# Performance work log

Hardware: AMD Instinct MI355X
Metric: run time of the kernel (lower is better)

Reference implementation:

```python
import jax, jax.numpy as jnp
import numpy as np

B = 4; N_LIG = 150; N_PROT = 550; N = 700
H = 128; HEADS = 4; KPH = 32; HPH = 32
L = 6; K = 48; EDGE_CH = 128; CUTOFF = 10.0
PROT_F = 27; NUM_CLASSES = 13
LOG2 = 0.6931471805599453
FLAT = N * H  # 89600, matches fc1 in_features


def ssp(x):
    # ShiftedSoftplus
    return jax.nn.softplus(x) - LOG2


def lin(x, w, b):
    # torch Linear convention: w is [out, in]
    return jnp.einsum('...i,oi->...o', x, w) + b


def setup_inputs() -> dict:
    key = jax.random.key(0)
    ki = iter(jax.random.split(key, 40))

    def nrm(shape, fan_in):
        return jax.random.normal(next(ki), shape, jnp.float32) / np.sqrt(fan_in).astype(np.float32)

    lig_pos = jax.random.normal(next(ki), (B, N_LIG, 3), jnp.float32) * 3.0
    lig_t = jax.random.randint(next(ki), (B, N_LIG, 1), 0, NUM_CLASSES).astype(jnp.float32)
    state = jnp.concatenate([lig_pos, lig_t], axis=-1)  # [B, N_LIG, 4]
    protein_pos_v = jnp.concatenate([
        jax.random.normal(next(ki), (B, N_PROT, 3), jnp.float32) * 3.0,
        jax.random.normal(next(ki), (B, N_PROT, PROT_F), jnp.float32)], axis=-1)  # [B, N_PROT, 30]

    inp = dict(state=state, protein_pos_v=protein_pos_v)
    inp['w_prot'] = nrm((H, PROT_F), PROT_F); inp['b_prot'] = jnp.zeros((H,), jnp.float32)
    inp['w_lig'] = nrm((H, NUM_CLASSES), NUM_CLASSES); inp['b_lig'] = jnp.zeros((H,), jnp.float32)
    # per-layer stacked encoder params (grouped 1x1 conv == per-head linear, no bias)
    inp['wq'] = nrm((L, HEADS, KPH, HPH), HPH)
    inp['wk'] = nrm((L, HEADS, KPH, HPH), HPH)
    inp['wv'] = nrm((L, HEADS, HPH, HPH), HPH)
    inp['wkn1_w'] = nrm((L, KPH, EDGE_CH), EDGE_CH); inp['wkn1_b'] = jnp.zeros((L, KPH), jnp.float32)
    inp['wkn2_w'] = nrm((L, KPH, KPH), KPH); inp['wkn2_b'] = jnp.zeros((L, KPH), jnp.float32)
    inp['wkl_w'] = nrm((L, KPH, KPH), KPH); inp['wkl_b'] = jnp.zeros((L, KPH), jnp.float32)
    inp['wvn1_w'] = nrm((L, HPH, EDGE_CH), EDGE_CH); inp['wvn1_b'] = jnp.zeros((L, HPH), jnp.float32)
    inp['wvn2_w'] = nrm((L, HPH, HPH), HPH); inp['wvn2_b'] = jnp.zeros((L, HPH), jnp.float32)
    inp['wvl_w'] = nrm((L, HPH, HPH), HPH); inp['wvl_b'] = jnp.zeros((L, HPH), jnp.float32)
    inp['cen_w'] = nrm((L, H, H), H); inp['cen_b'] = jnp.zeros((L, H), jnp.float32)
    inp['out_w'] = nrm((L, H, H), H); inp['out_b'] = jnp.zeros((L, H), jnp.float32)
    inp['ln_g'] = jnp.ones((L, H), jnp.float32); inp['ln_b'] = jnp.zeros((L, H), jnp.float32)
    inp['fc1_w'] = nrm((128, FLAT), FLAT); inp['fc1_b'] = jnp.zeros((128,), jnp.float32)
    inp['fc2_w'] = nrm((64, 128), 128); inp['fc2_b'] = jnp.zeros((64,), jnp.float32)
    inp['fc3_w'] = nrm((1, 64), 64); inp['fc3_b'] = jnp.zeros((1,), jnp.float32)
    return inp


def reference(state, protein_pos_v, w_prot, b_prot, w_lig, b_lig, wq, wk, wv,
              wkn1_w, wkn1_b, wkn2_w, wkn2_b, wkl_w, wkl_b,
              wvn1_w, wvn1_b, wvn2_w, wvn2_b, wvl_w, wvl_b,
              cen_w, cen_b, out_w, out_b, ln_g, ln_b,
              fc1_w, fc1_b, fc2_w, fc2_b, fc3_w, fc3_b):
    lig_pos = state[..., :3]
    lig_t = jax.lax.stop_gradient(state[..., 3]).astype(jnp.int32)
    lig_oh = jax.nn.one_hot(lig_t, NUM_CLASSES, dtype=jnp.float32)
    prot_pos = protein_pos_v[..., :3]
    prot_v = protein_pos_v[..., 3:]
    # compose_context: stable sort by batch -> protein atoms then ligand atoms per complex
    h = jnp.concatenate([lin(prot_v, w_prot, b_prot), lin(lig_oh, w_lig, b_lig)], axis=1)  # [B,N,H]
    pos = jnp.concatenate([prot_pos, lig_pos], axis=1)  # [B,N,3]
    # kNN graph (k nearest neighbors, no self loops), batched per complex
    d2 = jnp.sum((pos[:, :, None, :] - pos[:, None, :, :]) ** 2, axis=-1)  # [B,N,N]
    d2 = d2 + jnp.eye(N, dtype=d2.dtype) * 1e9
    _, nbr = jax.lax.top_k(-d2, K)  # [B,N,K]
    dist = jnp.sqrt(jnp.take_along_axis(d2, nbr, axis=2))  # [B,N,K]
    # Gaussian smearing of edge lengths
    offset = jnp.linspace(0.0, CUTOFF, EDGE_CH)
    coeff = -0.5 / (offset[1] - offset[0]) ** 2
    edge_attr = jnp.exp(coeff * (dist[..., None] - offset) ** 2)  # [B,N,K,E]
    gat = jax.vmap(lambda a, i: a[i])  # per-batch neighbor gather
    for l in range(L):
        xh = h.reshape(B, N, HEADS, HPH)
        q = jnp.einsum('bnhd,hkd->bnhk', xh, wq[l])
        kx = jnp.einsum('bnhd,hkd->bnhk', xh, wk[l])
        vx = jnp.einsum('bnhd,hkd->bnhk', xh, wv[l])
        w_k = lin(ssp(lin(edge_attr, wkn1_w[l], wkn1_b[l])), wkn2_w[l], wkn2_b[l])  # [B,N,K,KPH]
        keys_j = lin(w_k[:, :, :, None, :] * gat(kx, nbr), wkl_w[l], wkl_b[l])  # [B,N,K,heads,KPH]
        qk = jnp.einsum('bnhk,bnmhk->bnmh', q, keys_j)  # per-edge attention logits
        alpha = jax.nn.softmax(qk, axis=2)  # scatter_softmax over each node's K edges
        w_v = lin(ssp(lin(edge_attr, wvn1_w[l], wvn1_b[l])), wvn2_w[l], wvn2_b[l])  # [B,N,K,HPH]
        msg = lin(w_v[:, :, :, None, :] * gat(vx, nbr), wvl_w[l], wvl_b[l])  # [B,N,K,heads,HPH]
        aggr = jnp.einsum('bnmh,bnmhd->bnhd', alpha, msg).reshape(B, N, H)
        x = lin(h, cen_w[l], cen_b[l]) + aggr
        mu = jnp.mean(x, axis=-1, keepdims=True)
        var = jnp.var(x, axis=-1, keepdims=True)
        x = (x - mu) / jnp.sqrt(var + 1e-5) * ln_g[l] + ln_b[l]
        h = h + lin(ssp(x), out_w[l], out_b[l])  # residual per interaction block
    # decoup_batch + pad_tensor: constant 700 nodes/complex -> plain reshape
    x = h.reshape(B, FLAT)
    x = jax.nn.relu(lin(x, fc1_w, fc1_b))
    x = jax.nn.relu(lin(x, fc2_w, fc2_b))
    return lin(x, fc3_w, fc3_b)  # [B,1]
```

## Files before the change

### kernel.cpp

```cpp
#include <hip/hip_runtime.h>
#include <hip/hip_fp16.h>
#include <math.h>

constexpr int cB   = 4;
constexpr int cNL  = 150;
constexpr int cNP  = 550;
constexpr int cN   = 700;
constexpr int cH   = 128;
constexpr int cHeads = 4;
constexpr int cL   = 6;
constexpr int cK   = 48;
constexpr int cPF  = 27;
constexpr int cNC  = 13;
constexpr int cFLAT = cN * cH;
constexpr int cEdges = cB * cN * cK;

constexpr int   TABN = 4096;
#define TAB_DMAX 11.0f
#define TAB_HT   (TAB_DMAX / (float)(TABN - 1))
#define TAB_INV  ((float)(TABN - 1) / TAB_DMAX)

#define RBF_STEP (10.0f / 127.0f)
#define RBF_COEFF (-0.5f / (RBF_STEP * RBF_STEP))
#define LOG2F_C 0.69314718055994530942f

__device__ __forceinline__ float sspf(float x) {
    float ax = fabsf(x);
    return fmaxf(x, 0.0f) + __logf(1.0f + __expf(-ax)) - LOG2F_C;
}

__device__ __forceinline__ int mbcnt64(unsigned long long m) {
    return __builtin_amdgcn_mbcnt_hi((unsigned)(m >> 32),
           __builtin_amdgcn_mbcnt_lo((unsigned)m, 0));
}

__global__ void __launch_bounds__(256) k_init(
    const float* __restrict__ wq, const float* __restrict__ wk, const float* __restrict__ wv,
    const float* __restrict__ wkn1_w, const float* __restrict__ wvn1_w,
    const float* __restrict__ wkn2_w, const float* __restrict__ wvn2_w,
    const float* __restrict__ wvl_w,
    const float* __restrict__ cen_w, const float* __restrict__ out_w,
    float* __restrict__ wqT, float* __restrict__ wkT, float* __restrict__ wvT,
    float* __restrict__ w1Tk, float* __restrict__ w1Tv,
    float* __restrict__ w2Tk, float* __restrict__ w2Tv,
    float* __restrict__ wvlT,
    float* __restrict__ cenT, float* __restrict__ outT,
    const float* __restrict__ state, const float* __restrict__ ppv,
    const float* __restrict__ w_prot, const float* __restrict__ b_prot,
    const float* __restrict__ w_lig, const float* __restrict__ b_lig,
    float* __restrict__ h, float* __restrict__ pos)
{
    if (blockIdx.x < 1320) {
        int idx = blockIdx.x * 256 + threadIdx.x;
        if (idx < 3 * 24576) {
            int seg = idx / 24576, i = idx % 24576;
            const float* src = seg == 0 ? wq : (seg == 1 ? wk : wv);
            float* dst = seg == 0 ? wqT : (seg == 1 ? wkT : wvT);
            int l = i / 4096, r = i % 4096;
            int hh = r / 1024, r2 = r % 1024;
            int d = r2 / 32, k = r2 % 32;
            dst[i] = src[(((size_t)l * 4 + hh) * 32 + k) * 32 + d];
            return;
        }
        idx -= 3 * 24576;
        if (idx < 2 * 24576) {
            int seg = idx / 24576, i = idx % 24576;
            const float* src = seg == 0 ? wkn1_w : wvn1_w;
            float* dst = seg == 0 ? w1Tk : w1Tv;
            int l = i / 4096, r = i % 4096;
            int c = r / 32, o = r % 32;
            dst[i] = src[((size_t)l * 32 + o) * 128 + c];
            return;
        }
        idx -= 2 * 24576;
        if (idx < 3 * 6144) {
            int seg = idx / 6144, i = idx % 6144;
            const float* src = seg == 0 ? wkn2_w : (seg == 1 ? wvn2_w : wvl_w);
            float* dst = seg == 0 ? w2Tk : (seg == 1 ? w2Tv : wvlT);
            int l = i / 1024, r = i % 1024;
            int c = r / 32, o = r % 32;
            dst[i] = src[((size_t)l * 32 + o) * 32 + c];
            return;
        }
        idx -= 3 * 6144;
        int seg = idx / 98304, i = idx % 98304;
        const float* src = seg == 0 ? cen_w : out_w;
        float* dst = seg == 0 ? cenT : outT;
        int l = i / 16384, r = i % 16384;
        int ii = r / 128, o = r % 128;
        dst[i] = src[((size_t)l * 128 + o) * 128 + ii];
        return;
    }
    int rel = blockIdx.x - 1320;
    int node = rel * 2 + (threadIdx.x >> 7);
    int b = node / cN, n = node % cN;
    int o = threadIdx.x & 127;
    int lane = threadIdx.x & 63;
    float out;
    if (n < cNP) {
        const float* src = ppv + ((size_t)b * cNP + n) * 30;
        float v = (lane < 30) ? src[lane] : 0.f;
        float s = b_prot[o];
        #pragma unroll
        for (int f = 0; f < cPF; f++) s += w_prot[o * cPF + f] * __shfl(v, 3 + f);
        out = s;
        if (o < 3) pos[((size_t)b * cN + n) * 3 + o] = v;
    } else {
        int nl = n - cNP;
        const float* src = state + ((size_t)b * cNL + nl) * 4;
        float v = (lane < 4) ? src[lane] : 0.f;
        int t = (int)__shfl(v, 3);
        out = w_lig[o * cNC + t] + b_lig[o];
        if (o < 3) pos[((size_t)b * cN + n) * 3 + o] = v;
    }
    h[((size_t)b * cN + n) * cH + o] = out;
}

__global__ void __launch_bounds__(256) k_knn(
    const float* __restrict__ pos, int* __restrict__ nbr, float* __restrict__ dist,
    const float* __restrict__ w1Tk, const float* __restrict__ wkn1_b,
    const float* __restrict__ w2Tk, const float* __restrict__ wkn2_b,
    const float* __restrict__ w1Tv, const float* __restrict__ wvn1_b,
    const float* __restrict__ w2Tv, const float* __restrict__ wvn2_b,
    float* __restrict__ tabP,
    const float* __restrict__ hbuf,
    const float* __restrict__ wqT, const float* __restrict__ wkT, const float* __restrict__ wvT,
    float* __restrict__ q0, __half* __restrict__ kx0, __half* __restrict__ vx0)
{
    int tid = threadIdx.x;
    if (blockIdx.x < cN) {
        int lane = tid & 63;
        int node = blockIdx.x * 4 + (tid >> 6);
        int b = node / cN, n = node % cN;
        const float* pb = pos + (size_t)b * cN * 3;
        float px = pb[n * 3 + 0], py = pb[n * 3 + 1], pz = pb[n * 3 + 2];
        float d2v[11];
        #pragma unroll
        for (int s = 0; s < 11; s++) {
            int j = lane + s * 64;
            float d2 = 1e30f;
            if (j < cN) {
                float dx = pb[j * 3 + 0] - px;
                float dy = pb[j * 3 + 1] - py;
                float dz = pb[j * 3 + 2] - pz;
                d2 = dx * dx + dy * dy + dz * dz;
                if (j == n) d2 = 1e9f;
            }
            d2v[s] = d2;
        }
        unsigned p = 0;
        for (int bit = 30; bit >= 0; --bit) {
            unsigned t = p | (1u << bit);
            int cnt = 0;
            #pragma unroll
            for (int s = 0; s < 11; s++)
                cnt += __popcll(__ballot(__float_as_uint(d2v[s]) < t));
            if (cnt <= 47) p = t;
        }
        int c_lt = 0;
        #pragma unroll
        for (int s = 0; s < 11; s++)
            c_lt += __popcll(__ballot(__float_as_uint(d2v[s]) < p));
        int base = 0, ebase = c_lt, need = 48 - c_lt;
        #pragma unroll
        for (int s = 0; s < 11; s++) {
            unsigned u = __float_as_uint(d2v[s]);
            unsigned long long blt = __ballot(u < p);
            unsigned long long beq = __ballot(u == p);
            int posn = -1;
            int bl = mbcnt64(blt);
            if (u < p) posn = base + bl;
            base += __popcll(blt);
            int r = mbcnt64(beq);
            int cs = __popcll(beq);
            int take = need < cs ? need : cs;
            if (u == p && r < take) posn = ebase + r;
            ebase += take; need -= take;
            if (posn >= 0) {
                nbr[(size_t)node * cK + posn] = s * 64 + lane;
                dist[(size_t)node * cK + posn] = sqrtf(d2v[s]);
            }
        }
        return;
    }
    if (blockIdx.x < cN + TABN / 4) {
        int rel = blockIdx.x - cN;
        int lane = tid & 63;
        int e = rel * 4 + (tid >> 6);
        int side = lane >> 5, o = lane & 31;
        float d = (float)e * TAB_HT;
        float z = d * (127.0f / 10.0f);
        int c0 = (int)floorf(z) - 7;
        c0 = c0 < 0 ? 0 : (c0 > 112 ? 112 : c0);
        int i = lane & 15;
        float tt = d - RBF_STEP * (float)(c0 + i);
        float eav = __expf(RBF_COEFF * tt * tt);
        const float* w1T = (side ? w1Tv : w1Tk);
        const float* b1  = (side ? wvn1_b : wkn1_b);
        const float* w2T = (side ? w2Tv : w2Tk);
        const float* b2  = (side ? wvn2_b : wkn2_b);
        int srcb = side * 32;
        for (int l = 0; l < cL; l++) {
            float s = b1[l * 32 + o];
            const float* w1p = w1T + (size_t)l * 4096;
            #pragma unroll
            for (int ii = 0; ii < 16; ii++)
                s += w1p[(c0 + ii) * 32 + o] * __shfl(eav, ii);
            float t1 = sspf(s);
            float s2 = b2[l * 32 + o];
            const float* w2p = w2T + (size_t)l * 1024;
            #pragma unroll
            for (int cc = 0; cc < 32; cc++)
                s2 += w2p[cc * 32 + o] * __shfl(t1, srcb + cc);
            tabP[((((size_t)l * TABN + e) * 2 + side) * 32 + o) * 2] = s2;
            if (e > 0)
                tabP[((((size_t)l * TABN + (e - 1)) * 2 + side) * 32 + o) * 2 + 1] = s2;
        }
        return;
    }
    int bn = (blockIdx.x - cN - TABN / 4) * 2 + (tid >> 7);
    int o = tid & 127;
    int hh = o >> 5, kq = o & 31;
    float hval = hbuf[(size_t)bn * cH + o];
    size_t wo = ((size_t)0 * 4 + hh) * 1024;
    const float* bq = wqT + wo;
    const float* bk = wkT + wo;
    const float* bv = wvT + wo;
    int srcb = (hh & 1) * 32;
    float sq = 0.f, sk = 0.f, sv = 0.f;
    #pragma unroll
    for (int d = 0; d < 32; d++) {
        float x = __shfl(hval, srcb + d);
        sq += bq[d * 32 + kq] * x;
        sk += bk[d * 32 + kq] * x;
        sv += bv[d * 32 + kq] * x;
    }
    q0[(size_t)bn * cH + o] = sq;
    kx0[(size_t)bn * cH + o] = __float2half(sk);
    vx0[(size_t)bn * cH + o] = __float2half(sv);
}

__global__ void __launch_bounds__(128) k_attn(
    int l,
    const float* __restrict__ h_in, const float* __restrict__ qr,
    const __half* __restrict__ kxr, const __half* __restrict__ vxr,
    const int* __restrict__ nbr, const float* __restrict__ dist,
    const float* __restrict__ tabP,
    const float* __restrict__ wkl_w,
    const float* __restrict__ wvlT, const float* __restrict__ wvl_b,
    const float* __restrict__ cenT, const float* __restrict__ cen_b,
    const float* __restrict__ outT, const float* __restrict__ out_b,
    const float* __restrict__ ln_g, const float* __restrict__ ln_b,
    float* __restrict__ h_out,
    float* __restrict__ qw, __half* __restrict__ kxw, __half* __restrict__ vxw,
    const float* __restrict__ wqT, const float* __restrict__ wkT, const float* __restrict__ wvT)
{
    int o = threadIdx.x;
    int lane = o & 63;
    int bn = blockIdx.x;
    int b = bn / cN;
    int hh = o >> 5, c = o & 31;
    int srcb = (hh & 1) * 32;
    int hi = lane >> 5;

    __shared__ float sh_h[cH];
    __shared__ float sh_t[cH];
    __shared__ float sh_qk[cK * cHeads];
    __shared__ int   sh_nb[cK];
    __shared__ int   sh_idx[cK];
    __shared__ float sh_frac[cK];
    __shared__ float red[2][2];

    sh_h[o] = h_in[(size_t)bn * cH + o];
    float qv = qr[(size_t)bn * cH + o];
    if (o < cK) {
        sh_nb[o] = nbr[(size_t)bn * cK + o];
        float d = dist[(size_t)bn * cK + o];
        float z = d * TAB_INV;
        int idx = (int)z;
        if (idx > TABN - 2) idx = TABN - 2;
        sh_idx[o] = idx;
        sh_frac[o] = fminf(z - (float)idx, 1.0f);
    }
    __syncthreads();

    const float* wklp = wkl_w + l * 1024;
    float qt = 0.f;
    #pragma unroll 8
    for (int k = 0; k < 32; k++) qt += __shfl(qv, srcb + k) * wklp[k * 32 + c];

    const __half* kxb = kxr + (size_t)b * cN * cH;
    const __half* vxb = vxr + (size_t)b * cN * cH;
    const float2* tab2 = (const float2*)tabP + (size_t)l * TABN * 64;

    #pragma unroll 4
    for (int m = 0; m < cK; m += 2) {
        int j0 = sh_nb[m], j1 = sh_nb[m + 1];
        float k0 = __half2float(kxb[(size_t)j0 * cH + o]);
        float k1 = __half2float(kxb[(size_t)j1 * cH + o]);
        int mm = m + hi;
        float2 tp = tab2[((size_t)sh_idx[mm] * 2 + 0) * 32 + c];
        float wmine = tp.x + sh_frac[mm] * (tp.y - tp.x);
        float wother = __shfl_xor(wmine, 32);
        float w0 = hi ? wother : wmine;
        float w1 = hi ? wmine : wother;
        float pa = qt * w0 * k0;
        float pb = qt * w1 * k1;
        float x = (c & 1) ? pb : pa;
        float y = (c & 1) ? pa : pb;
        x += __shfl_xor(y, 1);
        x += __shfl_xor(x, 2);
        x += __shfl_xor(x, 4);
        x += __shfl_xor(x, 8);
        x += __shfl_xor(x, 16);
        if (c < 2) sh_qk[(m + c) * cHeads + hh] = x;
    }
    asm volatile("s_waitcnt lgkmcnt(0)" ::: "memory");

    {
        float v1 = sh_qk[c * cHeads + hh];
        float v2 = (c < cK - 32) ? sh_qk[(32 + c) * cHeads + hh] : -1e30f;
        float mx = fmaxf(v1, v2);
        #pragma unroll
        for (int off = 16; off; off >>= 1) mx = fmaxf(mx, __shfl_xor(mx, off));
        float e1 = __expf(v1 - mx);
        float e2 = (c < cK - 32) ? __expf(v2 - mx) : 0.f;
        float s = e1 + e2;
        #pragma unroll
        for (int off = 16; off; off >>= 1) s += __shfl_xor(s, off);
        float inv = 1.0f / s;
        sh_qk[c * cHeads + hh] = e1 * inv;
        if (c < cK - 32) sh_qk[(32 + c) * cHeads + hh] = e2 * inv;
    }
    asm volatile("s_waitcnt lgkmcnt(0)" ::: "memory");

    float t0 = 0.f, t1 = 0.f;
    #pragma unroll 4
    for (int m = 0; m < cK; m += 2) {
        int j0 = sh_nb[m], j1 = sh_nb[m + 1];
        float v0 = __half2float(vxb[(size_t)j0 * cH + o]);
        float v1 = __half2float(vxb[(size_t)j1 * cH + o]);
        int mm = m + hi;
        float2 sp = tab2[((size_t)sh_idx[mm] * 2 + 1) * 32 + c];
        float wmine = sp.x + sh_frac[mm] * (sp.y - sp.x);
        float wother = __shfl_xor(wmine, 32);
        float w0 = hi ? wother : wmine;
        float w1 = hi ? wmine : wother;
        t0 += sh_qk[m * cHeads + hh] * (w0 * v0);
        t1 += sh_qk[(m + 1) * cHeads + hh] * (w1 * v1);
    }
    float tt = t0 + t1;

    const float* wvlTp = wvlT + l * 1024;
    float aggr = wvl_b[l * 32 + c];
    #pragma unroll 8
    for (int i = 0; i < 32; i++) aggr += wvlTp[i * 32 + c] * __shfl(tt, srcb + i);

    const float* cenTp = cenT + (size_t)l * cH * cH;
    float x0 = 0.f, x1 = 0.f;
    #pragma unroll 4
    for (int i = 0; i < cH; i += 2) {
        x0 += cenTp[i * cH + o] * sh_h[i];
        x1 += cenTp[(i + 1) * cH + o] * sh_h[i + 1];
    }
    float x = cen_b[l * cH + o] + aggr + x0 + x1;

    float s1 = x, s2 = x * x;
    #pragma unroll
    for (int off = 32; off; off >>= 1) {
        s1 += __shfl_xor(s1, off);
        s2 += __shfl_xor(s2, off);
    }
    int wid = o >> 6;
    if (lane == 0) { red[wid][0] = s1; red[wid][1] = s2; }
    __syncthreads();
    float tot1 = red[0][0] + red[1][0], tot2 = red[0][1] + red[1][1];
    float mu = tot1 * (1.0f / 128.0f);
    float var = tot2 * (1.0f / 128.0f) - mu * mu;
    float xn = (x - mu) * rsqrtf(var + 1e-5f);
    xn = xn * ln_g[l * cH + o] + ln_b[l * cH + o];
    float sx = sspf(xn);
    sh_t[o] = sx;
    __syncthreads();

    const float* outTp = outT + (size_t)l * cH * cH;
    float o0 = 0.f, o1 = 0.f;
    #pragma unroll 4
    for (int i = 0; i < cH; i += 2) {
        o0 += outTp[i * cH + o] * sh_t[i];
        o1 += outTp[(i + 1) * cH + o] * sh_t[i + 1];
    }
    float hnew = sh_h[o] + out_b[l * cH + o] + o0 + o1;
    h_out[(size_t)bn * cH + o] = hnew;

    if (l < cL - 1) {
        size_t wo = ((size_t)(l + 1) * 4 + hh) * 1024;
        const float* bq = wqT + wo;
        const float* bk = wkT + wo;
        const float* bv = wvT + wo;
        float sq = 0.f, sk = 0.f, sv = 0.f;
        #pragma unroll
        for (int d = 0; d < 32; d++) {
            float xv = __shfl(hnew, srcb + d);
            sq += bq[d * 32 + c] * xv;
            sk += bk[d * 32 + c] * xv;
            sv += bv[d * 32 + c] * xv;
        }
        qw[(size_t)bn * cH + o] = sq;
        kxw[(size_t)bn * cH + o] = __float2half(sk);
        vxw[(size_t)bn * cH + o] = __float2half(sv);
    }
}

__global__ void __launch_bounds__(256) k_fc1p(const float* __restrict__ hbuf,
                                              const float* __restrict__ w,
                                              float* __restrict__ partial)
{
    int o = blockIdx.x >> 2, qp = blockIdx.x & 3;
    int tid = threadIdx.x;
    constexpr int CH = cFLAT / 4;
    const float4* wr = (const float4*)(w + (size_t)o * cFLAT + qp * CH);
    float a[4] = {0.f, 0.f, 0.f, 0.f};
    for (int i = tid; i < CH / 4; i += 256) {
        float4 wv = wr[i];
        #pragma unroll
        for (int bb = 0; bb < 4; bb++) {
            float4 hv = ((const float4*)(hbuf + (size_t)bb * cFLAT + qp * CH))[i];
            a[bb] += wv.x * hv.x + wv.y * hv.y + wv.z * hv.z + wv.w * hv.w;
        }
    }
    #pragma unroll
    for (int off = 32; off; off >>= 1) {
        #pragma unroll
        for (int bb = 0; bb < 4; bb++) a[bb] += __shfl_xor(a[bb], off);
    }
    __shared__ float red[4][4];
    if ((tid & 63) == 0) {
        #pragma unroll
        for (int bb = 0; bb < 4; bb++) red[tid >> 6][bb] = a[bb];
    }
    __syncthreads();
    if (tid < 4) {
        float s = red[0][tid] + red[1][tid] + red[2][tid] + red[3][tid];
        partial[((size_t)o * 4 + qp) * 4 + tid] = s;
    }
}

__global__ void __launch_bounds__(512) k_head2(const float* __restrict__ partial,
                                               const float* __restrict__ fc1_b,
                                               const float* __restrict__ fc2_w,
                                               const float* __restrict__ fc2_b,
                                               const float* __restrict__ fc3_w,
                                               const float* __restrict__ fc3_b,
                                               float* __restrict__ out)
{
    int tid = threadIdx.x;
    __shared__ float y1[4][128];
    __shared__ float y2[4][64];
    {
        int bb = tid >> 7, o = tid & 127;
        float s = fc1_b[o];
        #pragma unroll
        for (int qp = 0; qp < 4; qp++) s += partial[((size_t)o * 4 + qp) * 4 + bb];
        y1[bb][o] = fmaxf(s, 0.f);
    }
    __syncthreads();
    if (tid < 256) {
        int bb = tid >> 6, o = tid & 63;
        float s = fc2_b[o];
        #pragma unroll 8
        for (int i = 0; i < 128; i++) s += fc2_w[o * 128 + i] * y1[bb][i];
        y2[bb][o] = fmaxf(s, 0.f);
    }
    __syncthreads();
    if (tid < 4) {
        float s = fc3_b[0];
        #pragma unroll 8
        for (int i = 0; i < 64; i++) s += fc3_w[i] * y2[tid][i];
        out[tid] = s;
    }
}

extern "C" void kernel_launch(void* const* d_in, const int* in_sizes, int n_in,
                              void* d_out, int out_size, void* d_ws, size_t ws_size,
                              hipStream_t stream) {
    const float* state  = (const float*)d_in[0];
    const float* ppv    = (const float*)d_in[1];
    const float* w_prot = (const float*)d_in[2];
    const float* b_prot = (const float*)d_in[3];
    const float* w_lig  = (const float*)d_in[4];
    const float* b_lig  = (const float*)d_in[5];
    const float* wq     = (const float*)d_in[6];
    const float* wk     = (const float*)d_in[7];
    const float* wv     = (const float*)d_in[8];
    const float* wkn1_w = (const float*)d_in[9];
    const float* wkn1_b = (const float*)d_in[10];
    const float* wkn2_w = (const float*)d_in[11];
    const float* wkn2_b = (const float*)d_in[12];
    const float* wkl_w  = (const float*)d_in[13];
    const float* wvn1_w = (const float*)d_in[15];
    const float* wvn1_b = (const float*)d_in[16];
    const float* wvn2_w = (const float*)d_in[17];
    const float* wvn2_b = (const float*)d_in[18];
    const float* wvl_w  = (const float*)d_in[19];
    const float* wvl_b  = (const float*)d_in[20];
    const float* cen_w  = (const float*)d_in[21];
    const float* cen_b  = (const float*)d_in[22];
    const float* out_w  = (const float*)d_in[23];
    const float* out_b  = (const float*)d_in[24];
    const float* ln_g   = (const float*)d_in[25];
    const float* ln_b   = (const float*)d_in[26];
    const float* fc1_w  = (const float*)d_in[27];
    const float* fc1_b  = (const float*)d_in[28];
    const float* fc2_w  = (const float*)d_in[29];
    const float* fc2_b  = (const float*)d_in[30];
    const float* fc3_w  = (const float*)d_in[31];
    const float* fc3_b  = (const float*)d_in[32];

    float* ws = (float*)d_ws;
    size_t off = 0;
    float* pos   = ws + off; off += (size_t)cB * cN * 3;
    float* h_a   = ws + off; off += (size_t)cB * cN * cH;
    float* h_b   = ws + off; off += (size_t)cB * cN * cH;
    float* qA    = ws + off; off += (size_t)cB * cN * cH;
    float* qB    = ws + off; off += (size_t)cB * cN * cH;
    __half* kA   = (__half*)(ws + off); off += (size_t)cB * cN * cH / 2;
    __half* vA   = (__half*)(ws + off); off += (size_t)cB * cN * cH / 2;
    __half* kB   = (__half*)(ws + off); off += (size_t)cB * cN * cH / 2;
    __half* vB   = (__half*)(ws + off); off += (size_t)cB * cN * cH / 2;
    float* distb = ws + off; off += (size_t)cEdges;
    int*   nbrb  = (int*)(ws + off); off += (size_t)cEdges;
    float* tabb  = ws + off; off += (size_t)cL * TABN * 64 * 2;
    float* wqT   = ws + off; off += 24576;
    float* wkT   = ws + off; off += 24576;
    float* wvT   = ws + off; off += 24576;
    float* w1Tk  = ws + off; off += 24576;
    float* w1Tv  = ws + off; off += 24576;
    float* w2Tk  = ws + off; off += 6144;
    float* w2Tv  = ws + off; off += 6144;
    float* wvlT  = ws + off; off += 6144;
    float* cenT  = ws + off; off += 98304;
    float* outT  = ws + off; off += 98304;
    float* partial = ws + off; off += 2048;

    k_init<<<2720, 256, 0, stream>>>(wq, wk, wv, wkn1_w, wvn1_w, wkn2_w, wvn2_w,
                                     wvl_w, cen_w, out_w,
                                     wqT, wkT, wvT, w1Tk, w1Tv, w2Tk, w2Tv, wvlT, cenT, outT,
                                     state, ppv, w_prot, b_prot, w_lig, b_lig, h_a, pos);
    k_knn<<<cN + TABN / 4 + cB * cN / 2, 256, 0, stream>>>(
        pos, nbrb, distb,
        w1Tk, wkn1_b, w2Tk, wkn2_b, w1Tv, wvn1_b, w2Tv, wvn2_b, tabb,
        h_a, wqT, wkT, wvT, qA, kA, vA);

    float* hc = h_a;
    float* hn = h_b;
    for (int l = 0; l < cL; l++) {
        float* qr = (l & 1) ? qB : qA;
        __half* kr = (l & 1) ? kB : kA;
        __half* vr = (l & 1) ? vB : vA;
        float* qw2 = (l & 1) ? qA : qB;
        __half* kw2 = (l & 1) ? kA : kB;
        __half* vw2 = (l & 1) ? vA : vB;
        k_attn<<<cB * cN, 128, 0, stream>>>(l, hc, qr, kr, vr, nbrb, distb, tabb,
            wkl_w, wvlT, wvl_b, cenT, cen_b, outT, out_b, ln_g, ln_b,
            hn, qw2, kw2, vw2, wqT, wkT, wvT);
        float* tmp = hc; hc = hn; hn = tmp;
    }

    k_fc1p<<<512, 256, 0, stream>>>(hc, fc1_w, partial);
    k_head2<<<1, 512, 0, stream>>>(partial, fc1_b, fc2_w, fc2_b, fc3_w, fc3_b, (float*)d_out);
}
```

Baseline: 303.6 us.

## Split attention kernel into gather and node-batched dense kernels

The per-node attention kernel is split in two. A gather kernel computes the attention-weighted value sum per node and writes it to a buffer. A dense kernel then processes 16 nodes per block, so each weight load from the wvl, cen, out and next-layer qkv matrices is reused across 8 nodes per thread instead of being reloaded for every node. This cuts redundant weight traffic, but adds an extra kernel launch per layer and a round trip of the intermediate buffer through global memory.

```diff
diff --git a/kernel.cpp b/kernel.cpp
--- a/kernel.cpp
+++ b/kernel.cpp
@@ -240,20 +240,14 @@
     vx0[(size_t)bn * cH + o] = __float2half(sv);
 }
 
-__global__ void __launch_bounds__(128) k_attn(
+__global__ void __launch_bounds__(128) k_gather(
     int l,
-    const float* __restrict__ h_in, const float* __restrict__ qr,
+    const float* __restrict__ qr,
     const __half* __restrict__ kxr, const __half* __restrict__ vxr,
     const int* __restrict__ nbr, const float* __restrict__ dist,
     const float* __restrict__ tabP,
     const float* __restrict__ wkl_w,
-    const float* __restrict__ wvlT, const float* __restrict__ wvl_b,
-    const float* __restrict__ cenT, const float* __restrict__ cen_b,
-    const float* __restrict__ outT, const float* __restrict__ out_b,
-    const float* __restrict__ ln_g, const float* __restrict__ ln_b,
-    float* __restrict__ h_out,
-    float* __restrict__ qw, __half* __restrict__ kxw, __half* __restrict__ vxw,
-    const float* __restrict__ wqT, const float* __restrict__ wkT, const float* __restrict__ wvT)
+    float* __restrict__ tbuf)
 {
     int o = threadIdx.x;
     int lane = o & 63;
@@ -263,15 +257,11 @@
     int srcb = (hh & 1) * 32;
     int hi = lane >> 5;
 
-    __shared__ float sh_h[cH];
-    __shared__ float sh_t[cH];
     __shared__ float sh_qk[cK * cHeads];
     __shared__ int   sh_nb[cK];
     __shared__ int   sh_idx[cK];
     __shared__ float sh_frac[cK];
-    __shared__ float red[2][2];
-
-    sh_h[o] = h_in[(size_t)bn * cH + o];
+
     float qv = qr[(size_t)bn * cH + o];
     if (o < cK) {
         sh_nb[o] = nbr[(size_t)bn * cK + o];
@@ -349,66 +339,150 @@
         t0 += sh_qk[m * cHeads + hh] * (w0 * v0);
         t1 += sh_qk[(m + 1) * cHeads + hh] * (w1 * v1);
     }
-    float tt = t0 + t1;
-
-    const float* wvlTp = wvlT + l * 1024;
-    float aggr = wvl_b[l * 32 + c];
-    #pragma unroll 8
-    for (int i = 0; i < 32; i++) aggr += wvlTp[i * 32 + c] * __shfl(tt, srcb + i);
-
-    const float* cenTp = cenT + (size_t)l * cH * cH;
-    float x0 = 0.f, x1 = 0.f;
-    #pragma unroll 4
-    for (int i = 0; i < cH; i += 2) {
-        x0 += cenTp[i * cH + o] * sh_h[i];
-        x1 += cenTp[(i + 1) * cH + o] * sh_h[i + 1];
-    }
-    float x = cen_b[l * cH + o] + aggr + x0 + x1;
-
-    float s1 = x, s2 = x * x;
+    tbuf[(size_t)bn * cH + o] = t0 + t1;
+}
+
+__global__ void __launch_bounds__(256) k_dense(
+    int l,
+    const float* __restrict__ h_in, const float* __restrict__ tbuf,
+    const float* __restrict__ wvlT, const float* __restrict__ wvl_b,
+    const float* __restrict__ cenT, const float* __restrict__ cen_b,
+    const float* __restrict__ outT, const float* __restrict__ out_b,
+    const float* __restrict__ ln_g, const float* __restrict__ ln_b,
+    float* __restrict__ h_out,
+    float* __restrict__ qw, __half* __restrict__ kxw, __half* __restrict__ vxw,
+    const float* __restrict__ wqT, const float* __restrict__ wkT, const float* __restrict__ wvT)
+{
+    int tid = threadIdx.x;
+    int o = tid & 127, g = tid >> 7;
+    int hh = o >> 5, c = o & 31;
+    int n0 = g * 8;
+    size_t base = (size_t)blockIdx.x * 16 * cH;
+
+    __shared__ float sh_t[16][cH];
+    __shared__ float sh_h[16][cH];
+    __shared__ float sh_x[16][cH];
+    __shared__ float sh_sx[16][cH];
+    __shared__ float sh_hn[16][cH];
+    __shared__ float sh_st[16][2];
+
     #pragma unroll
-    for (int off = 32; off; off >>= 1) {
-        s1 += __shfl_xor(s1, off);
-        s2 += __shfl_xor(s2, off);
-    }
-    int wid = o >> 6;
-    if (lane == 0) { red[wid][0] = s1; red[wid][1] = s2; }
-    __syncthreads();
-    float tot1 = red[0][0] + red[1][0], tot2 = red[0][1] + red[1][1];
-    float mu = tot1 * (1.0f / 128.0f);
-    float var = tot2 * (1.0f / 128.0f) - mu * mu;
-    float xn = (x - mu) * rsqrtf(var + 1e-5f);
-    xn = xn * ln_g[l * cH + o] + ln_b[l * cH + o];
-    float sx = sspf(xn);
-    sh_t[o] = sx;
-    __syncthreads();
-
-    const float* outTp = outT + (size_t)l * cH * cH;
-    float o0 = 0.f, o1 = 0.f;
-    #pragma unroll 4
-    for (int i = 0; i < cH; i += 2) {
-        o0 += outTp[i * cH + o] * sh_t[i];
-        o1 += outTp[(i + 1) * cH + o] * sh_t[i + 1];
-    }
-    float hnew = sh_h[o] + out_b[l * cH + o] + o0 + o1;
-    h_out[(size_t)bn * cH + o] = hnew;
+    for (int s = 0; s < 8; s++) {
+        int f = tid + s * 256;
+        ((float*)sh_t)[f] = tbuf[base + f];
+        ((float*)sh_h)[f] = h_in[base + f];
+    }
+    __syncthreads();
+
+    float acc[8];
+    {
+        const float* wvlp = wvlT + l * 1024;
+        float wb = wvl_b[l * 32 + c];
+        #pragma unroll
+        for (int s = 0; s < 8; s++) acc[s] = wb;
+        #pragma unroll 4
+        for (int i = 0; i < 32; i++) {
+            float w = wvlp[i * 32 + c];
+            #pragma unroll
+            for (int s = 0; s < 8; s++) acc[s] += w * sh_t[n0 + s][hh * 32 + i];
+        }
+    }
+    {
+        const float* cenp = cenT + (size_t)l * cH * cH;
+        float cb = cen_b[l * cH + o];
+        #pragma unroll
+        for (int s = 0; s < 8; s++) acc[s] += cb;
+        #pragma unroll 4
+        for (int i = 0; i < cH; i++) {
+            float w = cenp[i * cH + o];
+            #pragma unroll
+            for (int s = 0; s < 8; s++) acc[s] += w * sh_h[n0 + s][i];
+        }
+        #pragma unroll
+        for (int s = 0; s < 8; s++) sh_x[n0 + s][o] = acc[s];
+    }
+    __syncthreads();
+
+    {
+        int n = tid >> 4, part = tid & 15;
+        float s1 = 0.f, s2 = 0.f;
+        #pragma unroll
+        for (int j = 0; j < 8; j++) {
+            float v = sh_x[n][part * 8 + j];
+            s1 += v; s2 += v * v;
+        }
+        #pragma unroll
+        for (int off = 8; off; off >>= 1) {
+            s1 += __shfl_xor(s1, off);
+            s2 += __shfl_xor(s2, off);
+        }
+        if (part == 0) {
+            float mu = s1 * (1.0f / 128.0f);
+            float var = s2 * (1.0f / 128.0f) - mu * mu;
+            sh_st[n][0] = mu;
+            sh_st[n][1] = rsqrtf(var + 1e-5f);
+        }
+    }
+    __syncthreads();
+
+    {
+        float gv = ln_g[l * cH + o], bv = ln_b[l * cH + o];
+        #pragma unroll
+        for (int s = 0; s < 8; s++) {
+            int n = n0 + s;
+            float xn = (sh_x[n][o] - sh_st[n][0]) * sh_st[n][1] * gv + bv;
+            sh_sx[n][o] = sspf(xn);
+        }
+    }
+    __syncthreads();
+
+    {
+        const float* outp = outT + (size_t)l * cH * cH;
+        float ob = out_b[l * cH + o];
+        #pragma unroll
+        for (int s = 0; s < 8; s++) acc[s] = ob + sh_h[n0 + s][o];
+        #pragma unroll 4
+        for (int i = 0; i < cH; i++) {
+            float w = outp[i * cH + o];
+            #pragma unroll
+            for (int s = 0; s < 8; s++) acc[s] += w * sh_sx[n0 + s][i];
+        }
+        #pragma unroll
+        for (int s = 0; s < 8; s++) {
+            sh_hn[n0 + s][o] = acc[s];
+            h_out[base + (size_t)(n0 + s) * cH + o] = acc[s];
+        }
+    }
+    __syncthreads();
 
     if (l < cL - 1) {
         size_t wo = ((size_t)(l + 1) * 4 + hh) * 1024;
         const float* bq = wqT + wo;
         const float* bk = wkT + wo;
         const float* bv = wvT + wo;
-        float sq = 0.f, sk = 0.f, sv = 0.f;
-        #pragma unroll
+        float aq[8], ak[8], av[8];
+        #pragma unroll
+        for (int s = 0; s < 8; s++) { aq[s] = 0.f; ak[s] = 0.f; av[s] = 0.f; }
+        #pragma unroll 4
         for (int d = 0; d < 32; d++) {
-            float xv = __shfl(hnew, srcb + d);
-            sq += bq[d * 32 + c] * xv;
-            sk += bk[d * 32 + c] * xv;
-            sv += bv[d * 32 + c] * xv;
-        }
-        qw[(size_t)bn * cH + o] = sq;
-        kxw[(size_t)bn * cH + o] = __float2half(sk);
-        vxw[(size_t)bn * cH + o] = __float2half(sv);
+            float wq_ = bq[d * 32 + c];
+            float wk_ = bk[d * 32 + c];
+            float wv_ = bv[d * 32 + c];
+            #pragma unroll
+            for (int s = 0; s < 8; s++) {
+                float hv = sh_hn[n0 + s][hh * 32 + d];
+                aq[s] += wq_ * hv;
+                ak[s] += wk_ * hv;
+                av[s] += wv_ * hv;
+            }
+        }
+        #pragma unroll
+        for (int s = 0; s < 8; s++) {
+            size_t p = base + (size_t)(n0 + s) * cH + o;
+            qw[p] = aq[s];
+            kxw[p] = __float2half(ak[s]);
+            vxw[p] = __float2half(av[s]);
+        }
     }
 }
 
@@ -531,6 +605,7 @@
     float* distb = ws + off; off += (size_t)cEdges;
     int*   nbrb  = (int*)(ws + off); off += (size_t)cEdges;
     float* tabb  = ws + off; off += (size_t)cL * TABN * 64 * 2;
+    float* tbuf  = ws + off; off += (size_t)cB * cN * cH;
     float* wqT   = ws + off; off += 24576;
     float* wkT   = ws + off; off += 24576;
     float* wvT   = ws + off; off += 24576;
@@ -561,8 +636,10 @@
         float* qw2 = (l & 1) ? qA : qB;
         __half* kw2 = (l & 1) ? kA : kB;
         __half* vw2 = (l & 1) ? vA : vB;
-        k_attn<<<cB * cN, 128, 0, stream>>>(l, hc, qr, kr, vr, nbrb, distb, tabb,
-            wkl_w, wvlT, wvl_b, cenT, cen_b, outT, out_b, ln_g, ln_b,
+        k_gather<<<cB * cN, 128, 0, stream>>>(l, qr, kr, vr, nbrb, distb, tabb,
+                                              wkl_w, tbuf);
+        k_dense<<<cB * cN / 16, 256, 0, stream>>>(l, hc, tbuf,
+            wvlT, wvl_b, cenT, cen_b, outT, out_b, ln_g, ln_b,
             hn, qw2, kw2, vw2, wqT, wkT, wvT);
         float* tmp = hc; hc = hn; hn = tmp;
     }
```

New measurement: 376.3 us. +23.9%, slower.
